# Optimization experiments

Measured on AMD Instinct MI355X. Metric: run time of the kernel, lower is better.

## Reference

```python
import jax, jax.numpy as jnp
import numpy as np
from jax import lax

DN = ('NCHW', 'OIHW', 'NCHW')


def setup_inputs() -> dict:
    key = jax.random.key(0)
    k1, k2 = jax.random.split(key)
    inp = jax.random.normal(k1, (32, 512, 28, 28), dtype=jnp.float32)
    w = jax.random.normal(k2, (2000, 512, 1, 1), dtype=jnp.float32)
    return {"input": inp, "weights": w}


def reference(input, weights):
    # conv2d(input^2, ones_like(weights)): every output channel is identical
    # (all-ones kernel broadcast over out-channels), so compute the
    # patch/channel sum ONCE with a single-output-channel ones kernel and
    # broadcast — same math as the original, without P-fold redundancy.
    P, C, kh, kw = weights.shape
    ones1 = jnp.ones((1, C, kh, kw), dtype=input.dtype)
    input2_patch_sum = lax.conv_general_dilated(
        input * input, ones1, window_strides=(1, 1), padding='VALID',
        dimension_numbers=DN)  # [B, 1, H', W'], broadcasts over P

    weights2 = jnp.sum(weights * weights, axis=(1, 2, 3))  # [P]
    weights2 = weights2.reshape(-1, 1, 1)  # [P, 1, 1]

    input_weights = lax.conv_general_dilated(
        input, weights, window_strides=(1, 1), padding='VALID',
        dimension_numbers=DN)  # [B, P, H', W']

    output = input2_patch_sum - 2.0 * input_weights + weights2[None]
    return jax.nn.relu(output)
```

## Files before the change

### kernel.cpp

```cpp
#include <hip/hip_runtime.h>
#include <stdint.h>

constexpr int C_IN  = 512;
constexpr int HW    = 784;
constexpr int NB    = 32;
constexpr int M_TOT = NB * HW;
constexpr int N_TOT = 2000;
constexpr int NPAD  = 2048;
constexpr int IMG_STRIDE = C_IN * HW;
constexpr int OUT_BATCH  = N_TOT * HW;

constexpr int TBM = 128;
constexpr int TBN = 128;
constexpr int NKT = C_IN / 32;

typedef __attribute__((ext_vector_type(8))) short bf16x8;
typedef __attribute__((ext_vector_type(4))) float f32x4;

__device__ __forceinline__ uint16_t f2bf(float f) {
    union { float f; uint32_t u; } x; x.f = f;
    return (uint16_t)((x.u + 0x8000u) >> 16);
}

__device__ __forceinline__ void gload_lds16(const void* g, void* l) {
    __builtin_amdgcn_global_load_lds(
        (const __attribute__((address_space(1))) void*)g,
        (__attribute__((address_space(3))) void*)l, 16, 0, 0);
}

__global__ __launch_bounds__(256) void prep_a_kernel(const float* __restrict__ in,
                                                     short* __restrict__ Abf,
                                                     float* __restrict__ s2) {
    __shared__ __align__(16) char T[64 * 512 * 2];
    __shared__ float red[16][64];

    const int t = threadIdx.x;
    const int q = t & 15;
    const int part = t >> 4;
    const int m0q = blockIdx.x * 64 + q * 4;
    const uint32_t b  = (uint32_t)m0q / 784u;
    const uint32_t hw = (uint32_t)m0q % 784u;
    const float* base = in + (size_t)b * IMG_STRIDE + hw;

    float4 acc = make_float4(0.f, 0.f, 0.f, 0.f);
    const int c0 = part * 32;
#pragma unroll 4
    for (int c = c0; c < c0 + 32; ++c) {
        float4 v = *(const float4*)(base + (size_t)c * HW);
        acc.x = fmaf(v.x, v.x, acc.x);
        acc.y = fmaf(v.y, v.y, acc.y);
        acc.z = fmaf(v.z, v.z, acc.z);
        acc.w = fmaf(v.w, v.w, acc.w);
        uint16_t vals[4] = { f2bf(v.x), f2bf(v.y), f2bf(v.z), f2bf(v.w) };
        const uint32_t by0 = (uint32_t)(q * 4) * 1024u + (uint32_t)c * 2u;
#pragma unroll
        for (int j = 0; j < 4; ++j) {
            uint32_t bb = by0 + (uint32_t)j * 1024u;
            bb ^= ((bb >> 12) & 7u) << 4;
            *(uint16_t*)(T + bb) = vals[j];
        }
    }
    red[part][q * 4 + 0] = acc.x;
    red[part][q * 4 + 1] = acc.y;
    red[part][q * 4 + 2] = acc.z;
    red[part][q * 4 + 3] = acc.w;
    __syncthreads();
    if (t < 64) {
        float s = 0.f;
#pragma unroll
        for (int p = 0; p < 16; ++p) s += red[p][t];
        s2[blockIdx.x * 64 + t] = s;
    }
    short* dst = Abf + (size_t)blockIdx.x * 64 * 512;
#pragma unroll
    for (int i = 0; i < 16; ++i) {
        const int idx = i * 256 + t;
        const int row = idx >> 6, ch = idx & 63;
        uint32_t bb = (uint32_t)row * 1024u + (uint32_t)ch * 16u;
        bb ^= ((bb >> 12) & 7u) << 4;
        bf16x8 v = *(bf16x8*)(T + bb);
        *(bf16x8*)(dst + (size_t)row * 512 + ch * 8) = v;
    }
}

__global__ __launch_bounds__(256) void prep_w_kernel(const float* __restrict__ w,
                                                     short* __restrict__ Wbf,
                                                     float* __restrict__ w2) {
    const int wv = threadIdx.x >> 6, lane = threadIdx.x & 63;
    const int p = blockIdx.x * 4 + wv;
    bf16x8 o = (bf16x8)0;
    float s = 0.f;
    if (p < N_TOT) {
        const float* base = w + (size_t)p * C_IN + lane * 8;
        float4 a = *(const float4*)base;
        float4 c = *(const float4*)(base + 4);
        s = a.x*a.x + a.y*a.y + a.z*a.z + a.w*a.w
          + c.x*c.x + c.y*c.y + c.z*c.z + c.w*c.w;
        o[0] = (short)f2bf(a.x); o[1] = (short)f2bf(a.y);
        o[2] = (short)f2bf(a.z); o[3] = (short)f2bf(a.w);
        o[4] = (short)f2bf(c.x); o[5] = (short)f2bf(c.y);
        o[6] = (short)f2bf(c.z); o[7] = (short)f2bf(c.w);
    }
    *(bf16x8*)(Wbf + (size_t)p * C_IN + lane * 8) = o;
#pragma unroll
    for (int off = 32; off; off >>= 1) s += __shfl_down(s, off);
    if (lane == 0) w2[p] = s;
}

__global__ __launch_bounds__(256, 3) void gemm5_kernel(const short* __restrict__ Abf,
                                                       const short* __restrict__ Wbf,
                                                       const float* __restrict__ s2,
                                                       const float* __restrict__ w2,
                                                       float* __restrict__ out) {
    __shared__ __align__(16) char smem[49152];

    const int t = threadIdx.x;
    const int wv = t >> 6, lane = t & 63;
    const int lr = lane & 15, lg = lane >> 4;

    const int bid = blockIdx.x;
    const int bn = bid & 15;
    const int bm = bid >> 4;

    const short* Ab = Abf + (size_t)bm * TBM * C_IN;
    const short* Bb = Wbf + (size_t)bn * TBN * C_IN;

    const int srow = wv * 32 + (lane >> 2);
    const int sg   = (lane & 3) ^ ((lane >> 3) & 3);
    const short* AsrcL = Ab + (size_t)srow * C_IN + sg * 8;
    const short* BsrcL = Bb + (size_t)srow * C_IN + sg * 8;
    const int adst = wv * 2048;

    const int wm = (wv >> 1) * 64;
    const int wn = (wv & 1) * 64;

    const int slot  = lg ^ ((lr >> 1) & 3);
    const int abase = (wm + lr) * 64 + slot * 16;
    const int bbase = 8192 + (wn + lr) * 64 + slot * 16;

    f32x4 acc[4][4] = {};

#define STAGE(tt)                                                              \
    do {                                                                       \
        char* buf_ = smem + ((tt) % 3) * 16384;                                \
        const short* As_ = AsrcL + (tt) * 32;                                  \
        const short* Bs_ = BsrcL + (tt) * 32;                                  \
        gload_lds16(As_,             buf_ + adst);                             \
        gload_lds16(As_ + 16 * 512,  buf_ + adst + 1024);                      \
        gload_lds16(Bs_,             buf_ + 8192 + adst);                      \
        gload_lds16(Bs_ + 16 * 512,  buf_ + 8192 + adst + 1024);               \
    } while (0)

    STAGE(0);
    STAGE(1);

#pragma unroll
    for (int kt = 0; kt < NKT; ++kt) {
        if (kt < NKT - 1) asm volatile("s_waitcnt vmcnt(4)" ::: "memory");
        else              asm volatile("s_waitcnt vmcnt(0)" ::: "memory");
        __builtin_amdgcn_sched_barrier(0);
        __builtin_amdgcn_s_barrier();
        __builtin_amdgcn_sched_barrier(0);

        if (kt + 2 < NKT) STAGE(kt + 2);

        const char* buf = smem + (kt % 3) * 16384;
        bf16x8 bfrag[4], afrag[4];
#pragma unroll
        for (int n = 0; n < 4; ++n)
            bfrag[n] = *(const bf16x8*)(buf + bbase + n * 1024);
#pragma unroll
        for (int m = 0; m < 4; ++m)
            afrag[m] = *(const bf16x8*)(buf + abase + m * 1024);

        __builtin_amdgcn_s_setprio(1);
#pragma unroll
        for (int m = 0; m < 4; ++m)
#pragma unroll
            for (int n = 0; n < 4; ++n)
                acc[m][n] = __builtin_amdgcn_mfma_f32_16x16x32_bf16(
                    afrag[m], bfrag[n], acc[m][n], 0, 0, 0);
        __builtin_amdgcn_s_setprio(0);
    }
#undef STAGE

#pragma unroll
    for (int m = 0; m < 4; ++m) {
        const int m_r = bm * TBM + wm + m * 16 + lg * 4;
        const float4 s2v = *(const float4*)(s2 + m_r);
        const uint32_t ob  = (uint32_t)m_r / 784u;
        const uint32_t ohw = (uint32_t)m_r % 784u;
        float* obase = out + (size_t)ob * OUT_BATCH + ohw;
#pragma unroll
        for (int n = 0; n < 4; ++n) {
            const int n_o = bn * TBN + wn + n * 16 + lr;
            if (n_o < N_TOT) {
                const float wvv = w2[n_o];
                const f32x4 a = acc[m][n];
                float4 r;
                r.x = fmaxf(s2v.x - 2.f * a.x + wvv, 0.f);
                r.y = fmaxf(s2v.y - 2.f * a.y + wvv, 0.f);
                r.z = fmaxf(s2v.z - 2.f * a.z + wvv, 0.f);
                r.w = fmaxf(s2v.w - 2.f * a.w + wvv, 0.f);
                *(float4*)(obase + (size_t)n_o * HW) = r;
            }
        }
    }
}

extern "C" void kernel_launch(void* const* d_in, const int* in_sizes, int n_in,
                              void* d_out, int out_size, void* d_ws, size_t ws_size,
                              hipStream_t stream) {
    const float* in = (const float*)d_in[0];
    const float* w  = (const float*)d_in[1];
    float* out = (float*)d_out;

    const size_t offA  = 0;
    const size_t offW  = offA + (size_t)M_TOT * C_IN * sizeof(short);
    const size_t offS2 = offW + (size_t)NPAD * C_IN * sizeof(short);
    const size_t offW2 = offS2 + (size_t)M_TOT * sizeof(float);

    short* Abf = (short*)((char*)d_ws + offA);
    short* Wbf = (short*)((char*)d_ws + offW);
    float* s2  = (float*)((char*)d_ws + offS2);
    float* w2  = (float*)((char*)d_ws + offW2);

    prep_a_kernel<<<M_TOT / 64, 256, 0, stream>>>(in, Abf, s2);
    prep_w_kernel<<<NPAD / 4, 256, 0, stream>>>(w, Wbf, w2);

    gemm5_kernel<<<196 * 16, 256, 0, stream>>>(Abf, Wbf, s2, w2, out);
}
```

Before: 109.6 us.

## Load weight fragments straight to registers and double the K-step per stage

The GEMM kernel stops staging the weight (B) tile through LDS. Each wave now loads its B fragments directly from global memory into double-buffered registers one K-step ahead. Only the activation tile still goes through a triple-buffered LDS pipeline, now with K=64 per stage and an 8-way XOR swizzle. This aims to cut LDS traffic and the number of barriers, at the cost of more VGPRs and uncoalesced, possibly redundant global B loads, since both waves sharing a wn range fetch the same B rows.

```diff
diff --git a/kernel.cpp b/kernel.cpp
--- a/kernel.cpp
+++ b/kernel.cpp
@@ -12,7 +12,7 @@
 
 constexpr int TBM = 128;
 constexpr int TBN = 128;
-constexpr int NKT = C_IN / 32;
+constexpr int NKT = C_IN / 64;
 
 typedef __attribute__((ext_vector_type(8))) short bf16x8;
 typedef __attribute__((ext_vector_type(4))) float f32x4;
@@ -107,7 +107,7 @@
     if (lane == 0) w2[p] = s;
 }
 
-__global__ __launch_bounds__(256, 3) void gemm5_kernel(const short* __restrict__ Abf,
+__global__ __launch_bounds__(256, 3) void gemm6_kernel(const short* __restrict__ Abf,
                                                        const short* __restrict__ Wbf,
                                                        const float* __restrict__ s2,
                                                        const float* __restrict__ w2,
@@ -123,36 +123,74 @@
     const int bm = bid >> 4;
 
     const short* Ab = Abf + (size_t)bm * TBM * C_IN;
-    const short* Bb = Wbf + (size_t)bn * TBN * C_IN;
-
-    const int srow = wv * 32 + (lane >> 2);
-    const int sg   = (lane & 3) ^ ((lane >> 3) & 3);
-    const short* AsrcL = Ab + (size_t)srow * C_IN + sg * 8;
-    const short* BsrcL = Bb + (size_t)srow * C_IN + sg * 8;
-    const int adst = wv * 2048;
+
+    const int arow = wv * 8 + (lane >> 3);
+    const int ag   = (lane & 7) ^ ((lane >> 3) & 7);
+    const short* AsrcL = Ab + (size_t)arow * C_IN + ag * 8;
+    const int adst = wv * 1024;
 
     const int wm = (wv >> 1) * 64;
     const int wn = (wv & 1) * 64;
 
-    const int slot  = lg ^ ((lr >> 1) & 3);
-    const int abase = (wm + lr) * 64 + slot * 16;
-    const int bbase = 8192 + (wn + lr) * 64 + slot * 16;
-
+    const int ab0 = (wm + lr) * 128 + ((lg ^ (lr & 7)) * 16);
+    const int ab1 = ab0 ^ 64;
+
+    const short* Bq0 = Wbf + (size_t)(bn * TBN + wn + lr) * C_IN + lg * 8;
+    const short* Bq1 = Bq0 + 16 * C_IN;
+    const short* Bq2 = Bq0 + 32 * C_IN;
+    const short* Bq3 = Bq0 + 48 * C_IN;
+
+    bf16x8 b0[4][2], b1[4][2];
     f32x4 acc[4][4] = {};
 
-#define STAGE(tt)                                                              \
+#define LOADB(tt, arr)                                                         \
+    do {                                                                       \
+        arr[0][0] = *(const bf16x8*)(Bq0 + (tt) * 64);                         \
+        arr[0][1] = *(const bf16x8*)(Bq0 + (tt) * 64 + 32);                    \
+        arr[1][0] = *(const bf16x8*)(Bq1 + (tt) * 64);                         \
+        arr[1][1] = *(const bf16x8*)(Bq1 + (tt) * 64 + 32);                    \
+        arr[2][0] = *(const bf16x8*)(Bq2 + (tt) * 64);                         \
+        arr[2][1] = *(const bf16x8*)(Bq2 + (tt) * 64 + 32);                    \
+    } while (0);                                                               \
+    do {                                                                       \
+        arr[3][0] = *(const bf16x8*)(Bq3 + (tt) * 64);                         \
+        arr[3][1] = *(const bf16x8*)(Bq3 + (tt) * 64 + 32);                    \
+    } while (0)
+
+#define STAGEA(tt)                                                             \
     do {                                                                       \
         char* buf_ = smem + ((tt) % 3) * 16384;                                \
-        const short* As_ = AsrcL + (tt) * 32;                                  \
-        const short* Bs_ = BsrcL + (tt) * 32;                                  \
-        gload_lds16(As_,             buf_ + adst);                             \
-        gload_lds16(As_ + 16 * 512,  buf_ + adst + 1024);                      \
-        gload_lds16(Bs_,             buf_ + 8192 + adst);                      \
-        gload_lds16(Bs_ + 16 * 512,  buf_ + 8192 + adst + 1024);               \
+        const short* s_ = AsrcL + (tt) * 64;                                   \
+        gload_lds16(s_,            buf_ + adst);                               \
+        gload_lds16(s_ + 32 * 512, buf_ + adst + 4096);                        \
+        gload_lds16(s_ + 64 * 512, buf_ + adst + 8192);                        \
+        gload_lds16(s_ + 96 * 512, buf_ + adst + 12288);                       \
     } while (0)
 
-    STAGE(0);
-    STAGE(1);
+#define COMPUTE(bb)                                                            \
+    do {                                                                       \
+        bf16x8 af[4];                                                          \
+        _Pragma("unroll") for (int m = 0; m < 4; ++m)                          \
+            af[m] = *(const bf16x8*)(buf + ab0 + m * 2048);                    \
+        __builtin_amdgcn_s_setprio(1);                                         \
+        _Pragma("unroll") for (int m = 0; m < 4; ++m)                          \
+            _Pragma("unroll") for (int n = 0; n < 4; ++n)                      \
+                acc[m][n] = __builtin_amdgcn_mfma_f32_16x16x32_bf16(           \
+                    af[m], bb[n][0], acc[m][n], 0, 0, 0);                      \
+        __builtin_amdgcn_s_setprio(0);                                         \
+        _Pragma("unroll") for (int m = 0; m < 4; ++m)                          \
+            af[m] = *(const bf16x8*)(buf + ab1 + m * 2048);                    \
+        __builtin_amdgcn_s_setprio(1);                                         \
+        _Pragma("unroll") for (int m = 0; m < 4; ++m)                          \
+            _Pragma("unroll") for (int n = 0; n < 4; ++n)                      \
+                acc[m][n] = __builtin_amdgcn_mfma_f32_16x16x32_bf16(           \
+                    af[m], bb[n][1], acc[m][n], 0, 0, 0);                      \
+        __builtin_amdgcn_s_setprio(0);                                         \
+    } while (0)
+
+    LOADB(0, b0);
+    STAGEA(0);
+    STAGEA(1);
 
 #pragma unroll
     for (int kt = 0; kt < NKT; ++kt) {
@@ -162,27 +200,19 @@
         __builtin_amdgcn_s_barrier();
         __builtin_amdgcn_sched_barrier(0);
 
-        if (kt + 2 < NKT) STAGE(kt + 2);
+        if (kt + 1 < NKT) {
+            if (kt & 1) { LOADB(kt + 1, b0); }
+            else        { LOADB(kt + 1, b1); }
+        }
+        if (kt + 2 < NKT) STAGEA(kt + 2);
 
         const char* buf = smem + (kt % 3) * 16384;
-        bf16x8 bfrag[4], afrag[4];
-#pragma unroll
-        for (int n = 0; n < 4; ++n)
-            bfrag[n] = *(const bf16x8*)(buf + bbase + n * 1024);
-#pragma unroll
-        for (int m = 0; m < 4; ++m)
-            afrag[m] = *(const bf16x8*)(buf + abase + m * 1024);
-
-        __builtin_amdgcn_s_setprio(1);
-#pragma unroll
-        for (int m = 0; m < 4; ++m)
-#pragma unroll
-            for (int n = 0; n < 4; ++n)
-                acc[m][n] = __builtin_amdgcn_mfma_f32_16x16x32_bf16(
-                    afrag[m], bfrag[n], acc[m][n], 0, 0, 0);
-        __builtin_amdgcn_s_setprio(0);
-    }
-#undef STAGE
+        if (kt & 1) { COMPUTE(b1); }
+        else        { COMPUTE(b0); }
+    }
+#undef LOADB
+#undef STAGEA
+#undef COMPUTE
 
 #pragma unroll
     for (int m = 0; m < 4; ++m) {
@@ -228,5 +258,5 @@
     prep_a_kernel<<<M_TOT / 64, 256, 0, stream>>>(in, Abf, s2);
     prep_w_kernel<<<NPAD / 4, 256, 0, stream>>>(w, Wbf, w2);
 
-    gemm5_kernel<<<196 * 16, 256, 0, stream>>>(Abf, Wbf, s2, w2, out);
-}
+    gemm6_kernel<<<196 * 16, 256, 0, stream>>>(Abf, Wbf, s2, w2, out);
+}
```

Result: slower. 152.5 us (+39.2%).

## Merge prep kernels into one launch and double-buffer GEMM for higher occupancy

Applied to the files above, without the earlier changes.

The input and weight preprocessing kernels are fused into a single launch, with the weight-conversion path taken by extra blocks. The GEMM drops from a triple-buffered LDS pipeline (48KB) to a double-buffered one (32KB) with launch bounds raised from 3 to 5 blocks per CU, aiming for more resident waves. The cost is less prefetch depth: each k-step now waits on its next tile's loads and adds a full barrier per iteration. Register pressure under the tighter launch bound may also cause spills.

```diff
diff --git a/kernel.cpp b/kernel.cpp
--- a/kernel.cpp
+++ b/kernel.cpp
@@ -14,6 +14,9 @@
 constexpr int TBN = 128;
 constexpr int NKT = C_IN / 32;
 
+constexpr int PREPA_BLOCKS = M_TOT / 64;
+constexpr int PREPW_BLOCKS = NPAD / 4;
+
 typedef __attribute__((ext_vector_type(8))) short bf16x8;
 typedef __attribute__((ext_vector_type(4))) float f32x4;
 
@@ -28,13 +31,40 @@
         (__attribute__((address_space(3))) void*)l, 16, 0, 0);
 }
 
-__global__ __launch_bounds__(256) void prep_a_kernel(const float* __restrict__ in,
-                                                     short* __restrict__ Abf,
-                                                     float* __restrict__ s2) {
+__global__ __launch_bounds__(256) void prep_kernel(const float* __restrict__ in,
+                                                   const float* __restrict__ w,
+                                                   short* __restrict__ Abf,
+                                                   short* __restrict__ Wbf,
+                                                   float* __restrict__ s2,
+                                                   float* __restrict__ w2) {
     __shared__ __align__(16) char T[64 * 512 * 2];
     __shared__ float red[16][64];
 
     const int t = threadIdx.x;
+
+    if (blockIdx.x >= PREPA_BLOCKS) {
+        const int wv = t >> 6, lane = t & 63;
+        const int p = (blockIdx.x - PREPA_BLOCKS) * 4 + wv;
+        bf16x8 o = (bf16x8)0;
+        float s = 0.f;
+        if (p < N_TOT) {
+            const float* base = w + (size_t)p * C_IN + lane * 8;
+            float4 a = *(const float4*)base;
+            float4 c = *(const float4*)(base + 4);
+            s = a.x*a.x + a.y*a.y + a.z*a.z + a.w*a.w
+              + c.x*c.x + c.y*c.y + c.z*c.z + c.w*c.w;
+            o[0] = (short)f2bf(a.x); o[1] = (short)f2bf(a.y);
+            o[2] = (short)f2bf(a.z); o[3] = (short)f2bf(a.w);
+            o[4] = (short)f2bf(c.x); o[5] = (short)f2bf(c.y);
+            o[6] = (short)f2bf(c.z); o[7] = (short)f2bf(c.w);
+        }
+        *(bf16x8*)(Wbf + (size_t)p * C_IN + lane * 8) = o;
+#pragma unroll
+        for (int off = 32; off; off >>= 1) s += __shfl_down(s, off);
+        if (lane == 0) w2[p] = s;
+        return;
+    }
+
     const int q = t & 15;
     const int part = t >> 4;
     const int m0q = blockIdx.x * 64 + q * 4;
@@ -83,36 +113,12 @@
     }
 }
 
-__global__ __launch_bounds__(256) void prep_w_kernel(const float* __restrict__ w,
-                                                     short* __restrict__ Wbf,
-                                                     float* __restrict__ w2) {
-    const int wv = threadIdx.x >> 6, lane = threadIdx.x & 63;
-    const int p = blockIdx.x * 4 + wv;
-    bf16x8 o = (bf16x8)0;
-    float s = 0.f;
-    if (p < N_TOT) {
-        const float* base = w + (size_t)p * C_IN + lane * 8;
-        float4 a = *(const float4*)base;
-        float4 c = *(const float4*)(base + 4);
-        s = a.x*a.x + a.y*a.y + a.z*a.z + a.w*a.w
-          + c.x*c.x + c.y*c.y + c.z*c.z + c.w*c.w;
-        o[0] = (short)f2bf(a.x); o[1] = (short)f2bf(a.y);
-        o[2] = (short)f2bf(a.z); o[3] = (short)f2bf(a.w);
-        o[4] = (short)f2bf(c.x); o[5] = (short)f2bf(c.y);
-        o[6] = (short)f2bf(c.z); o[7] = (short)f2bf(c.w);
-    }
-    *(bf16x8*)(Wbf + (size_t)p * C_IN + lane * 8) = o;
-#pragma unroll
-    for (int off = 32; off; off >>= 1) s += __shfl_down(s, off);
-    if (lane == 0) w2[p] = s;
-}
-
-__global__ __launch_bounds__(256, 3) void gemm5_kernel(const short* __restrict__ Abf,
+__global__ __launch_bounds__(256, 5) void gemm7_kernel(const short* __restrict__ Abf,
                                                        const short* __restrict__ Wbf,
                                                        const float* __restrict__ s2,
                                                        const float* __restrict__ w2,
                                                        float* __restrict__ out) {
-    __shared__ __align__(16) char smem[49152];
+    __shared__ __align__(16) char smem[32768];
 
     const int t = threadIdx.x;
     const int wv = t >> 6, lane = t & 63;
@@ -142,7 +148,7 @@
 
 #define STAGE(tt)                                                              \
     do {                                                                       \
-        char* buf_ = smem + ((tt) % 3) * 16384;                                \
+        char* buf_ = smem + ((tt) & 1) * 16384;                                \
         const short* As_ = AsrcL + (tt) * 32;                                  \
         const short* Bs_ = BsrcL + (tt) * 32;                                  \
         gload_lds16(As_,             buf_ + adst);                             \
@@ -152,19 +158,16 @@
     } while (0)
 
     STAGE(0);
-    STAGE(1);
+    asm volatile("s_waitcnt vmcnt(0)" ::: "memory");
+    __builtin_amdgcn_sched_barrier(0);
+    __builtin_amdgcn_s_barrier();
+    __builtin_amdgcn_sched_barrier(0);
 
 #pragma unroll
     for (int kt = 0; kt < NKT; ++kt) {
-        if (kt < NKT - 1) asm volatile("s_waitcnt vmcnt(4)" ::: "memory");
-        else              asm volatile("s_waitcnt vmcnt(0)" ::: "memory");
-        __builtin_amdgcn_sched_barrier(0);
-        __builtin_amdgcn_s_barrier();
-        __builtin_amdgcn_sched_barrier(0);
-
-        if (kt + 2 < NKT) STAGE(kt + 2);
-
-        const char* buf = smem + (kt % 3) * 16384;
+        if (kt + 1 < NKT) STAGE(kt + 1);
+
+        const char* buf = smem + (kt & 1) * 16384;
         bf16x8 bfrag[4], afrag[4];
 #pragma unroll
         for (int n = 0; n < 4; ++n)
@@ -181,6 +184,13 @@
                 acc[m][n] = __builtin_amdgcn_mfma_f32_16x16x32_bf16(
                     afrag[m], bfrag[n], acc[m][n], 0, 0, 0);
         __builtin_amdgcn_s_setprio(0);
+
+        if (kt + 1 < NKT) {
+            asm volatile("s_waitcnt vmcnt(0) lgkmcnt(0)" ::: "memory");
+            __builtin_amdgcn_sched_barrier(0);
+            __builtin_amdgcn_s_barrier();
+            __builtin_amdgcn_sched_barrier(0);
+        }
     }
 #undef STAGE
 
@@ -225,8 +235,7 @@
     float* s2  = (float*)((char*)d_ws + offS2);
     float* w2  = (float*)((char*)d_ws + offW2);
 
-    prep_a_kernel<<<M_TOT / 64, 256, 0, stream>>>(in, Abf, s2);
-    prep_w_kernel<<<NPAD / 4, 256, 0, stream>>>(w, Wbf, w2);
-
-    gemm5_kernel<<<196 * 16, 256, 0, stream>>>(Abf, Wbf, s2, w2, out);
-}
+    prep_kernel<<<PREPA_BLOCKS + PREPW_BLOCKS, 256, 0, stream>>>(in, w, Abf, Wbf, s2, w2);
+
+    gemm7_kernel<<<196 * 16, 256, 0, stream>>>(Abf, Wbf, s2, w2, out);
+}
```

New measurement: 257.9 us. 135% more time.
